# Performance work log

Hardware: AMD Instinct MI355X
Metric: run time of the kernel (lower is better)

The kernel has to match this reference:

```python
import jax, jax.numpy as jnp
import numpy as np

B, S = 8, 512          # batch, seq_len
D, F = 1024, 2048      # d_model, head hidden dim
H = 16                 # num_tasks (= num heads)
V = 3000               # selfies vocab
O = 1                  # head output size
INIT = 0.02


def setup_inputs() -> dict:
    key = jax.random.key(0)
    ks = jax.random.split(key, 12)
    return {
        "selfies": jax.random.randint(ks[0], (B, S), 0, V),
        "tasks": jax.random.randint(ks[1], (B, S), 0, H + 1),  # 0 -> invalid (-1)
        "values": jax.random.normal(ks[2], (B, S), jnp.float32),
        "property_mask": jax.random.randint(ks[3], (B, S), 0, 2).astype(bool),
        # shared_base params (embed + FFN -> [B,S,D])
        "emb_selfies": jax.random.normal(ks[4], (V, D), jnp.float32) * INIT,
        "emb_tasks": jax.random.normal(ks[5], (H + 1, D), jnp.float32) * INIT,
        "val_vec": jax.random.normal(ks[6], (D,), jnp.float32) * INIT,
        "Ws": jax.random.normal(ks[7], (D, D), jnp.float32) * INIT,
        "bs": jnp.zeros((D,), jnp.float32),
        # stacked per-head MLP params: Linear(D,F) -> GELU -> Linear(F,O)
        "W1": jax.random.normal(ks[8], (H, D, F), jnp.float32) * INIT,
        "b1": jnp.zeros((H, F), jnp.float32),
        "W2": jax.random.normal(ks[9], (H, F, O), jnp.float32) * INIT,
        "b2": jnp.zeros((H, O), jnp.float32),
    }


def reference(selfies, tasks, values, property_mask,
              emb_selfies, emb_tasks, val_vec, Ws, bs, W1, b1, W2, b2):
    # ---- shared_base: embed + masked token features + FFN -> [B,S,D] ----
    h = (emb_selfies[selfies] + emb_tasks[tasks] + values[..., None] * val_vec)
    h = h * property_mask[..., None].astype(h.dtype)
    shared = jax.nn.gelu(h @ Ws + bs)                      # [B,S,D]

    # ---- routing: task token -> head index, 0 means invalid (-1) ----
    head_idx = jnp.where(tasks > 0, (tasks - 1) % H, -1)   # [B,S]

    # ---- each active head runs its MLP over the FULL shared_output ----
    hid = jax.nn.gelu(jnp.einsum('bsd,hdf->bshf', shared, W1) + b1)  # [B,S,H,F]
    heads_out = jnp.einsum('bshf,hfo->bsho', hid, W2) + b2           # [B,S,H,O]

    # ---- scatter/select per token by head index; invalid -> zeros ----
    idx = jnp.clip(head_idx, 0)
    out = jnp.take_along_axis(heads_out, idx[..., None, None], axis=2)[:, :, 0, :]
    return jnp.where(head_idx[..., None] >= 0, out, jnp.zeros_like(out))
```

## Files before the change

kernel.cpp:

```cpp
#include <hip/hip_runtime.h>
#include <hip/hip_bf16.h>

#define TOK 4096
#define DD  1024
#define FF  2048
#define NH  16

typedef short bf16x8 __attribute__((ext_vector_type(8)));
typedef float f32x4  __attribute__((ext_vector_type(4)));

__device__ __forceinline__ float gelu_f(float x) {
  float u = 0.7978845608028654f * (x + 0.044715f * x * x * x);
  float e = __expf(2.0f * u);
  return 0.5f * x * (2.0f - 2.0f / (e + 1.0f));
}

__device__ __forceinline__ unsigned short f2bf(float f) {
  union { float f; unsigned u; } v; v.f = f;
  unsigned r = v.u + 0x7FFF + ((v.u >> 16) & 1);
  return (unsigned short)(r >> 16);
}
__device__ __forceinline__ unsigned pack2(float a, float b) {
  return (unsigned)f2bf(a) | ((unsigned)f2bf(b) << 16);
}

__device__ __forceinline__ void load_lds16(const void* g, void* l) {
  __builtin_amdgcn_global_load_lds(
      (const __attribute__((address_space(1))) void*)g,
      (__attribute__((address_space(3))) void*)l, 16, 0, 0);
}

__global__ __launch_bounds__(256) void route_kernel(
    const int* __restrict__ tasks, const float* __restrict__ b2,
    int* __restrict__ counts, int* __restrict__ lists, float* __restrict__ out) {
  int t = blockIdx.x * 256 + threadIdx.x;
  if (t >= TOK) return;
  int task = tasks[t];
  if (task > 0) {
    int h = (task - 1) & (NH - 1);
    int pos = atomicAdd(&counts[h], 1);
    lists[h * TOK + pos] = t;
    out[t] = b2[h];
  } else {
    out[t] = 0.0f;
  }
}

__global__ __launch_bounds__(256) void prep_x(
    const int* __restrict__ selfies, const int* __restrict__ tasks,
    const float* __restrict__ values, const int* __restrict__ pmask,
    const float* __restrict__ emb_s, const float* __restrict__ emb_t,
    const float* __restrict__ val_vec, unsigned short* __restrict__ Xb) {
  int gid = blockIdx.x * 256 + threadIdx.x;
  int kc = (gid & 127) * 8;
  int t  = gid >> 7;
  int sid = selfies[t], tsk = tasks[t];
  float v = values[t];
  float msk = pmask[t] ? 1.0f : 0.0f;
  const float* ps = emb_s + (size_t)sid * DD + kc;
  const float* pt = emb_t + (size_t)tsk * DD + kc;
  const float* pv = val_vec + kc;
  float r[8];
#pragma unroll
  for (int j = 0; j < 8; j += 4) {
    float4 a = *(const float4*)(ps + j);
    float4 b = *(const float4*)(pt + j);
    float4 c = *(const float4*)(pv + j);
    r[j + 0] = (a.x + b.x + v * c.x) * msk;
    r[j + 1] = (a.y + b.y + v * c.y) * msk;
    r[j + 2] = (a.z + b.z + v * c.z) * msk;
    r[j + 3] = (a.w + b.w + v * c.w) * msk;
  }
  uint4 o;
  o.x = pack2(r[0], r[1]); o.y = pack2(r[2], r[3]);
  o.z = pack2(r[4], r[5]); o.w = pack2(r[6], r[7]);
  *(uint4*)(Xb + (size_t)gid * 8) = o;
}

#define W1_TILES (16 * 16 * 32)
#define WS_TILES (16 * 16)

__global__ __launch_bounds__(256) void prep_w(
    const float* __restrict__ Ws, const float* __restrict__ W1,
    unsigned short* __restrict__ Wsp, unsigned short* __restrict__ W1p) {
  __shared__ unsigned short T[64][70];
  int bid = blockIdx.x;
  const float* src; unsigned short* dstBase; int stride, nt0, kc0;
  if (bid < W1_TILES) {
    int fb = bid & 31, kb = (bid >> 5) & 15, h = bid >> 9;
    src = W1 + ((size_t)h * DD + kb * 64) * FF + fb * 64;
    stride = FF;
    nt0 = h * 128 + fb * 4;
    kc0 = kb * 2;
    dstBase = W1p;
  } else {
    int b2 = bid - W1_TILES;
    int fb = b2 & 15, kb = b2 >> 4;
    src = Ws + (size_t)(kb * 64) * DD + fb * 64;
    stride = DD;
    nt0 = fb * 4;
    kc0 = kb * 2;
    dstBase = Wsp;
  }
  const int tid = threadIdx.x;
  {
    int r = tid >> 2, cq = (tid & 3) * 16;
    const float* p = src + (size_t)r * stride + cq;
#pragma unroll
    for (int i = 0; i < 4; ++i) {
      float4 v = *(const float4*)(p + i * 4);
      *(unsigned*)&T[r][cq + i * 4 + 0] = pack2(v.x, v.y);
      *(unsigned*)&T[r][cq + i * 4 + 2] = pack2(v.z, v.w);
    }
  }
  __syncthreads();
#pragma unroll
  for (int cc = 0; cc < 2; ++cc) {
    int idx = tid + cc * 256;
    int lane2 = idx & 63, kcl = (idx >> 6) & 1, ntl = idx >> 7;
    int n_local = ntl * 16 + (lane2 & 15);
    int r0 = kcl * 32 + (lane2 >> 4) * 8;
    unsigned short e[8];
#pragma unroll
    for (int j = 0; j < 8; ++j) e[j] = T[r0 + j][n_local];
    uint4 o;
    o.x = (unsigned)e[0] | ((unsigned)e[1] << 16);
    o.y = (unsigned)e[2] | ((unsigned)e[3] << 16);
    o.z = (unsigned)e[4] | ((unsigned)e[5] << 16);
    o.w = (unsigned)e[6] | ((unsigned)e[7] << 16);
    size_t chunk = ((size_t)(nt0 + ntl) * 32 + (kc0 + kcl)) * 64 + lane2;
    *(uint4*)(dstBase + chunk * 8) = o;
  }
}

__global__ __launch_bounds__(256) void gemm1_mfma(
    const unsigned short* __restrict__ Xb, const unsigned short* __restrict__ Wsp,
    const float* __restrict__ bs, unsigned short* __restrict__ shared_bf) {
  __shared__ __align__(16) unsigned short As[2][2 * 4 * 64 * 8];
  __shared__ __align__(16) unsigned short Bs[2][2 * 8 * 64 * 8];

  const int tid = threadIdx.x;
  const int lane = tid & 63, w = tid >> 6;
  const int m0 = blockIdx.x * 64;
  const int n0 = blockIdx.y * 128;
  const int q = lane >> 4, c = lane & 15;

  const unsigned short* aSrc = Xb + (size_t)(m0 + w * 16 + c) * DD + q * 8;
  const unsigned short* bBase = Wsp + ((size_t)(blockIdx.y * 8 + w * 2)) * 32 * 512 + lane * 8;
  f32x4 acc[4][2] = {};

  float bsv[2];
  bsv[0] = bs[n0 + w * 32 + c];
  bsv[1] = bs[n0 + w * 32 + 16 + c];
  asm volatile("" :: "v"(bsv[0]), "v"(bsv[1]));

  auto stage = [&](int buf, int k0) {
    load_lds16(aSrc + k0,      As[buf] + (size_t)(0 * 256 + w * 64 + lane) * 8);
    load_lds16(aSrc + k0 + 32, As[buf] + (size_t)(1 * 256 + w * 64 + lane) * 8);
    const unsigned short* bk = bBase + k0 * 16;
#pragma unroll
    for (int i = 0; i < 4; ++i) {
      int kk = i >> 1, t = i & 1;
      load_lds16(bk + (size_t)t * 16384 + kk * 512,
                 Bs[buf] + (size_t)(kk * 8 + w * 2 + t) * 512 + lane * 8);
    }
  };
  auto compute = [&](int buf) {
#pragma unroll
    for (int kk = 0; kk < 2; ++kk) {
      bf16x8 a[4], b[2];
#pragma unroll
      for (int mt = 0; mt < 4; ++mt)
        a[mt] = *(const bf16x8*)(As[buf] + (size_t)((kk * 4 + mt) * 64 + lane) * 8);
#pragma unroll
      for (int t = 0; t < 2; ++t)
        b[t] = *(const bf16x8*)(Bs[buf] + (size_t)((kk * 8 + w * 2 + t) * 64 + lane) * 8);
#pragma unroll
      for (int mt = 0; mt < 4; ++mt)
#pragma unroll
        for (int t = 0; t < 2; ++t)
          acc[mt][t] = __builtin_amdgcn_mfma_f32_16x16x32_bf16(a[mt], b[t], acc[mt][t], 0, 0, 0);
    }
  };

  stage(0, 0);
  stage(1, 64);
  asm volatile("s_waitcnt vmcnt(6)" ::: "memory");
  __builtin_amdgcn_s_barrier();
  int cur = 0;
  for (int i = 0; i < 14; ++i) {
    compute(cur);
    asm volatile("" ::: "memory");
    __builtin_amdgcn_s_barrier();
    stage(cur, (i + 2) * 64);
    asm volatile("s_waitcnt vmcnt(6)" ::: "memory");
    __builtin_amdgcn_s_barrier();
    cur ^= 1;
  }
  compute(cur);
  asm volatile("s_waitcnt vmcnt(0)" ::: "memory");
  __builtin_amdgcn_s_barrier();
  compute(cur ^ 1);

#pragma unroll
  for (int mt = 0; mt < 4; ++mt)
#pragma unroll
    for (int t = 0; t < 2; ++t)
#pragma unroll
      for (int r = 0; r < 4; ++r) {
        int row = m0 + mt * 16 + q * 4 + r;
        int col = n0 + w * 32 + t * 16 + c;
        shared_bf[(size_t)row * DD + col] = f2bf(gelu_f(acc[mt][t][r] + bsv[t]));
      }
}

__global__ __launch_bounds__(256) void gemm2_mfma(
    const unsigned short* __restrict__ shared_bf, const unsigned short* __restrict__ W1p,
    const float* __restrict__ b1, const float* __restrict__ W2,
    const int* __restrict__ counts, const int* __restrict__ lists,
    float* __restrict__ out) {
  const int id = blockIdx.x;
  const int xcd = id & 7, local_ = id >> 3;
  const int h = xcd + 8 * (local_ >> 7);
  const int rest = local_ & 127;
  const int fc = rest & 15;
  const int m0 = (rest >> 4) * 64;
  const int nt_h = counts[h];
  if (m0 >= nt_h) return;

  __shared__ __align__(16) unsigned short As[2][2 * 4 * 64 * 8];
  __shared__ __align__(16) unsigned short Bs[2][2 * 8 * 64 * 8];
  __shared__ int   stok[64];
  __shared__ float red[4][68];

  const int tid = threadIdx.x;
  const int lane = tid & 63, w = tid >> 6;
  const int q = lane >> 4, c = lane & 15;

  if (tid < 64) {
    int i = m0 + tid;
    stok[tid] = (i < nt_h) ? lists[h * TOK + i] : -1;
  }
  __syncthreads();

  int tokr = stok[w * 16 + c];
  if (tokr < 0) tokr = 0;
  const unsigned short* aSrc = shared_bf + (size_t)tokr * DD + q * 8;
  const unsigned short* bBase =
      W1p + ((size_t)h * 128 + fc * 8 + w * 2) * 32 * 512 + lane * 8;

  f32x4 acc[4][2] = {};

  const float* b1h = b1 + (size_t)h * FF + fc * 128 + w * 32;
  const float* w2h = W2 + (size_t)h * FF + fc * 128 + w * 32;
  float b1v[2], w2v[2];
  b1v[0] = b1h[c];      b1v[1] = b1h[16 + c];
  w2v[0] = w2h[c];      w2v[1] = w2h[16 + c];
  asm volatile("" :: "v"(b1v[0]), "v"(b1v[1]), "v"(w2v[0]), "v"(w2v[1]));

  auto stage = [&](int buf, int k0) {
    load_lds16(aSrc + k0,      As[buf] + (size_t)(0 * 256 + w * 64 + lane) * 8);
    load_lds16(aSrc + k0 + 32, As[buf] + (size_t)(1 * 256 + w * 64 + lane) * 8);
    const unsigned short* bk = bBase + k0 * 16;
#pragma unroll
    for (int i = 0; i < 4; ++i) {
      int kk = i >> 1, t = i & 1;
      load_lds16(bk + (size_t)t * 16384 + kk * 512,
                 Bs[buf] + (size_t)(kk * 8 + w * 2 + t) * 512 + lane * 8);
    }
  };
  auto compute = [&](int buf) {
#pragma unroll
    for (int kk = 0; kk < 2; ++kk) {
      bf16x8 a[4], b[2];
#pragma unroll
      for (int mt = 0; mt < 4; ++mt)
        a[mt] = *(const bf16x8*)(As[buf] + (size_t)((kk * 4 + mt) * 64 + lane) * 8);
#pragma unroll
      for (int t = 0; t < 2; ++t)
        b[t] = *(const bf16x8*)(Bs[buf] + (size_t)((kk * 8 + w * 2 + t) * 64 + lane) * 8);
#pragma unroll
      for (int mt = 0; mt < 4; ++mt)
#pragma unroll
        for (int t = 0; t < 2; ++t)
          acc[mt][t] = __builtin_amdgcn_mfma_f32_16x16x32_bf16(a[mt], b[t], acc[mt][t], 0, 0, 0);
    }
  };

  stage(0, 0);
  stage(1, 64);
  asm volatile("s_waitcnt vmcnt(6)" ::: "memory");
  __builtin_amdgcn_s_barrier();
  int cur = 0;
  for (int i = 0; i < 14; ++i) {
    compute(cur);
    asm volatile("" ::: "memory");
    __builtin_amdgcn_s_barrier();
    stage(cur, (i + 2) * 64);
    asm volatile("s_waitcnt vmcnt(6)" ::: "memory");
    __builtin_amdgcn_s_barrier();
    cur ^= 1;
  }
  compute(cur);
  asm volatile("s_waitcnt vmcnt(0)" ::: "memory");
  __builtin_amdgcn_s_barrier();
  compute(cur ^ 1);

#pragma unroll
  for (int mt = 0; mt < 4; ++mt)
#pragma unroll
    for (int r = 0; r < 4; ++r) {
      float s = 0.0f;
#pragma unroll
      for (int t = 0; t < 2; ++t)
        s += gelu_f(acc[mt][t][r] + b1v[t]) * w2v[t];
      s += __shfl_xor(s, 1);
      s += __shfl_xor(s, 2);
      s += __shfl_xor(s, 4);
      s += __shfl_xor(s, 8);
      if (c == 0) red[w][mt * 16 + q * 4 + r] = s;
    }
  __syncthreads();

  if (tid < 64) {
    int t = stok[tid];
    if (t >= 0) {
      float s = red[0][tid] + red[1][tid] + red[2][tid] + red[3][tid];
      atomicAdd(&out[t], s);
    }
  }
}

extern "C" void kernel_launch(void* const* d_in, const int* in_sizes, int n_in,
                              void* d_out, int out_size, void* d_ws, size_t ws_size,
                              hipStream_t stream) {
  const int*   selfies = (const int*)d_in[0];
  const int*   tasks   = (const int*)d_in[1];
  const float* values  = (const float*)d_in[2];
  const int*   pmask   = (const int*)d_in[3];
  const float* emb_s   = (const float*)d_in[4];
  const float* emb_t   = (const float*)d_in[5];
  const float* val_vec = (const float*)d_in[6];
  const float* Ws      = (const float*)d_in[7];
  const float* bs      = (const float*)d_in[8];
  const float* W1      = (const float*)d_in[9];
  const float* b1      = (const float*)d_in[10];
  const float* W2      = (const float*)d_in[11];
  const float* b2      = (const float*)d_in[12];
  float* out = (float*)d_out;

  char* ws = (char*)d_ws;
  unsigned short* Xb        = (unsigned short*)ws;
  unsigned short* shared_bf = (unsigned short*)(ws + (8u << 20));
  unsigned short* Wsp       = (unsigned short*)(ws + (16u << 20));
  unsigned short* W1p       = (unsigned short*)(ws + (18u << 20));
  int* counts = (int*)(ws + (82u << 20));
  int* lists  = (int*)(ws + (82u << 20) + 256);

  hipMemsetAsync(counts, 0, NH * sizeof(int), stream);
  route_kernel<<<TOK / 256, 256, 0, stream>>>(tasks, b2, counts, lists, out);
  prep_x<<<TOK * 128 / 256, 256, 0, stream>>>(selfies, tasks, values, pmask,
                                              emb_s, emb_t, val_vec, Xb);
  prep_w<<<W1_TILES + WS_TILES, 256, 0, stream>>>(Ws, W1, Wsp, W1p);
  gemm1_mfma<<<dim3(TOK / 64, DD / 128), 256, 0, stream>>>(Xb, Wsp, bs, shared_bf);
  gemm2_mfma<<<2048, 256, 0, stream>>>(shared_bf, W1p, b1, W2,
                                       counts, lists, out);
}
```

Measured before the change: 320.2 us.

## Merge prep kernels into one launch and deepen GEMM pipelines to four stages

Fuses the routing, activation-prep and weight-prep kernels into a single launch that dispatches on block index, removing two kernel launches and their gaps. Both MFMA GEMMs switch from a 2-buffer, 64-wide K step to a 4-buffer, 32-wide K step with one barrier per iteration and loads issued two steps ahead. MFMA sections are wrapped in s_setprio to favour the math waves. The deeper ring hides more global latency but halves the work per barrier, and the LDS footprint stays the same.

```diff
diff --git a/kernel.cpp b/kernel.cpp
--- a/kernel.cpp
+++ b/kernel.cpp
@@ -30,61 +30,15 @@
       (__attribute__((address_space(3))) void*)l, 16, 0, 0);
 }
 
-__global__ __launch_bounds__(256) void route_kernel(
-    const int* __restrict__ tasks, const float* __restrict__ b2,
-    int* __restrict__ counts, int* __restrict__ lists, float* __restrict__ out) {
-  int t = blockIdx.x * 256 + threadIdx.x;
-  if (t >= TOK) return;
-  int task = tasks[t];
-  if (task > 0) {
-    int h = (task - 1) & (NH - 1);
-    int pos = atomicAdd(&counts[h], 1);
-    lists[h * TOK + pos] = t;
-    out[t] = b2[h];
-  } else {
-    out[t] = 0.0f;
-  }
-}
-
-__global__ __launch_bounds__(256) void prep_x(
-    const int* __restrict__ selfies, const int* __restrict__ tasks,
-    const float* __restrict__ values, const int* __restrict__ pmask,
-    const float* __restrict__ emb_s, const float* __restrict__ emb_t,
-    const float* __restrict__ val_vec, unsigned short* __restrict__ Xb) {
-  int gid = blockIdx.x * 256 + threadIdx.x;
-  int kc = (gid & 127) * 8;
-  int t  = gid >> 7;
-  int sid = selfies[t], tsk = tasks[t];
-  float v = values[t];
-  float msk = pmask[t] ? 1.0f : 0.0f;
-  const float* ps = emb_s + (size_t)sid * DD + kc;
-  const float* pt = emb_t + (size_t)tsk * DD + kc;
-  const float* pv = val_vec + kc;
-  float r[8];
-#pragma unroll
-  for (int j = 0; j < 8; j += 4) {
-    float4 a = *(const float4*)(ps + j);
-    float4 b = *(const float4*)(pt + j);
-    float4 c = *(const float4*)(pv + j);
-    r[j + 0] = (a.x + b.x + v * c.x) * msk;
-    r[j + 1] = (a.y + b.y + v * c.y) * msk;
-    r[j + 2] = (a.z + b.z + v * c.z) * msk;
-    r[j + 3] = (a.w + b.w + v * c.w) * msk;
-  }
-  uint4 o;
-  o.x = pack2(r[0], r[1]); o.y = pack2(r[2], r[3]);
-  o.z = pack2(r[4], r[5]); o.w = pack2(r[6], r[7]);
-  *(uint4*)(Xb + (size_t)gid * 8) = o;
-}
-
 #define W1_TILES (16 * 16 * 32)
 #define WS_TILES (16 * 16)
-
-__global__ __launch_bounds__(256) void prep_w(
-    const float* __restrict__ Ws, const float* __restrict__ W1,
+#define PW_BLKS  (W1_TILES + WS_TILES)
+#define PX_BLKS  (TOK * 128 / 256)
+
+__device__ void prep_w_body(
+    int bid, const float* __restrict__ Ws, const float* __restrict__ W1,
     unsigned short* __restrict__ Wsp, unsigned short* __restrict__ W1p) {
   __shared__ unsigned short T[64][70];
-  int bid = blockIdx.x;
   const float* src; unsigned short* dstBase; int stride, nt0, kc0;
   if (bid < W1_TILES) {
     int fb = bid & 31, kb = (bid >> 5) & 15, h = bid >> 9;
@@ -133,11 +87,72 @@
   }
 }
 
+__device__ void prep_x_body(
+    int gid, const int* __restrict__ selfies, const int* __restrict__ tasks,
+    const float* __restrict__ values, const int* __restrict__ pmask,
+    const float* __restrict__ emb_s, const float* __restrict__ emb_t,
+    const float* __restrict__ val_vec, unsigned short* __restrict__ Xb) {
+  int kc = (gid & 127) * 8;
+  int t  = gid >> 7;
+  int sid = selfies[t], tsk = tasks[t];
+  float v = values[t];
+  float msk = pmask[t] ? 1.0f : 0.0f;
+  const float* ps = emb_s + (size_t)sid * DD + kc;
+  const float* pt = emb_t + (size_t)tsk * DD + kc;
+  const float* pv = val_vec + kc;
+  float r[8];
+#pragma unroll
+  for (int j = 0; j < 8; j += 4) {
+    float4 a = *(const float4*)(ps + j);
+    float4 b = *(const float4*)(pt + j);
+    float4 c = *(const float4*)(pv + j);
+    r[j + 0] = (a.x + b.x + v * c.x) * msk;
+    r[j + 1] = (a.y + b.y + v * c.y) * msk;
+    r[j + 2] = (a.z + b.z + v * c.z) * msk;
+    r[j + 3] = (a.w + b.w + v * c.w) * msk;
+  }
+  uint4 o;
+  o.x = pack2(r[0], r[1]); o.y = pack2(r[2], r[3]);
+  o.z = pack2(r[4], r[5]); o.w = pack2(r[6], r[7]);
+  *(uint4*)(Xb + (size_t)gid * 8) = o;
+}
+
+__global__ __launch_bounds__(256) void prep_all(
+    const int* __restrict__ selfies, const int* __restrict__ tasks,
+    const float* __restrict__ values, const int* __restrict__ pmask,
+    const float* __restrict__ emb_s, const float* __restrict__ emb_t,
+    const float* __restrict__ val_vec, const float* __restrict__ Ws,
+    const float* __restrict__ W1, const float* __restrict__ b2,
+    unsigned short* __restrict__ Xb, unsigned short* __restrict__ Wsp,
+    unsigned short* __restrict__ W1p,
+    int* __restrict__ counts, int* __restrict__ lists, float* __restrict__ out) {
+  int bid = blockIdx.x;
+  if (bid < PW_BLKS) {
+    prep_w_body(bid, Ws, W1, Wsp, W1p);
+  } else if (bid < PW_BLKS + PX_BLKS) {
+    prep_x_body((bid - PW_BLKS) * 256 + threadIdx.x,
+                selfies, tasks, values, pmask, emb_s, emb_t, val_vec, Xb);
+  } else {
+    int t = (bid - PW_BLKS - PX_BLKS) * 256 + threadIdx.x;
+    if (t < TOK) {
+      int task = tasks[t];
+      if (task > 0) {
+        int h = (task - 1) & (NH - 1);
+        int pos = atomicAdd(&counts[h], 1);
+        lists[h * TOK + pos] = t;
+        out[t] = b2[h];
+      } else {
+        out[t] = 0.0f;
+      }
+    }
+  }
+}
+
 __global__ __launch_bounds__(256) void gemm1_mfma(
     const unsigned short* __restrict__ Xb, const unsigned short* __restrict__ Wsp,
     const float* __restrict__ bs, unsigned short* __restrict__ shared_bf) {
-  __shared__ __align__(16) unsigned short As[2][2 * 4 * 64 * 8];
-  __shared__ __align__(16) unsigned short Bs[2][2 * 8 * 64 * 8];
+  __shared__ __align__(16) unsigned short As[4][4 * 64 * 8];
+  __shared__ __align__(16) unsigned short Bs[4][8 * 64 * 8];
 
   const int tid = threadIdx.x;
   const int lane = tid & 63, w = tid >> 6;
@@ -154,53 +169,45 @@
   bsv[1] = bs[n0 + w * 32 + 16 + c];
   asm volatile("" :: "v"(bsv[0]), "v"(bsv[1]));
 
-  auto stage = [&](int buf, int k0) {
-    load_lds16(aSrc + k0,      As[buf] + (size_t)(0 * 256 + w * 64 + lane) * 8);
-    load_lds16(aSrc + k0 + 32, As[buf] + (size_t)(1 * 256 + w * 64 + lane) * 8);
-    const unsigned short* bk = bBase + k0 * 16;
-#pragma unroll
-    for (int i = 0; i < 4; ++i) {
-      int kk = i >> 1, t = i & 1;
-      load_lds16(bk + (size_t)t * 16384 + kk * 512,
-                 Bs[buf] + (size_t)(kk * 8 + w * 2 + t) * 512 + lane * 8);
-    }
+  auto stage = [&](int buf, int kc2) {
+    load_lds16(aSrc + kc2 * 32, As[buf] + (size_t)(w * 64 + lane) * 8);
+    const unsigned short* bk = bBase + kc2 * 512;
+    load_lds16(bk,            Bs[buf] + (size_t)((w * 2 + 0) * 64 + lane) * 8);
+    load_lds16(bk + 16384,    Bs[buf] + (size_t)((w * 2 + 1) * 64 + lane) * 8);
   };
   auto compute = [&](int buf) {
-#pragma unroll
-    for (int kk = 0; kk < 2; ++kk) {
-      bf16x8 a[4], b[2];
-#pragma unroll
-      for (int mt = 0; mt < 4; ++mt)
-        a[mt] = *(const bf16x8*)(As[buf] + (size_t)((kk * 4 + mt) * 64 + lane) * 8);
+    bf16x8 a[4], b[2];
+#pragma unroll
+    for (int mt = 0; mt < 4; ++mt)
+      a[mt] = *(const bf16x8*)(As[buf] + (size_t)(mt * 64 + lane) * 8);
+#pragma unroll
+    for (int t = 0; t < 2; ++t)
+      b[t] = *(const bf16x8*)(Bs[buf] + (size_t)((w * 2 + t) * 64 + lane) * 8);
+    __builtin_amdgcn_s_setprio(1);
+#pragma unroll
+    for (int mt = 0; mt < 4; ++mt)
 #pragma unroll
       for (int t = 0; t < 2; ++t)
-        b[t] = *(const bf16x8*)(Bs[buf] + (size_t)((kk * 8 + w * 2 + t) * 64 + lane) * 8);
-#pragma unroll
-      for (int mt = 0; mt < 4; ++mt)
-#pragma unroll
-        for (int t = 0; t < 2; ++t)
-          acc[mt][t] = __builtin_amdgcn_mfma_f32_16x16x32_bf16(a[mt], b[t], acc[mt][t], 0, 0, 0);
-    }
+        acc[mt][t] = __builtin_amdgcn_mfma_f32_16x16x32_bf16(a[mt], b[t], acc[mt][t], 0, 0, 0);
+    __builtin_amdgcn_s_setprio(0);
   };
 
   stage(0, 0);
-  stage(1, 64);
-  asm volatile("s_waitcnt vmcnt(6)" ::: "memory");
-  __builtin_amdgcn_s_barrier();
-  int cur = 0;
-  for (int i = 0; i < 14; ++i) {
-    compute(cur);
-    asm volatile("" ::: "memory");
-    __builtin_amdgcn_s_barrier();
-    stage(cur, (i + 2) * 64);
+  stage(1, 1);
+  for (int i = 0; i < 30; ++i) {
+    stage((i + 2) & 3, i + 2);
     asm volatile("s_waitcnt vmcnt(6)" ::: "memory");
     __builtin_amdgcn_s_barrier();
-    cur ^= 1;
-  }
-  compute(cur);
+    compute(i & 3);
+    asm volatile("" ::: "memory");
+  }
+  asm volatile("s_waitcnt vmcnt(3)" ::: "memory");
+  __builtin_amdgcn_s_barrier();
+  compute(2);
+  asm volatile("" ::: "memory");
   asm volatile("s_waitcnt vmcnt(0)" ::: "memory");
   __builtin_amdgcn_s_barrier();
-  compute(cur ^ 1);
+  compute(3);
 
 #pragma unroll
   for (int mt = 0; mt < 4; ++mt)
@@ -228,8 +235,8 @@
   const int nt_h = counts[h];
   if (m0 >= nt_h) return;
 
-  __shared__ __align__(16) unsigned short As[2][2 * 4 * 64 * 8];
-  __shared__ __align__(16) unsigned short Bs[2][2 * 8 * 64 * 8];
+  __shared__ __align__(16) unsigned short As[4][4 * 64 * 8];
+  __shared__ __align__(16) unsigned short Bs[4][8 * 64 * 8];
   __shared__ int   stok[64];
   __shared__ float red[4][68];
 
@@ -258,53 +265,45 @@
   w2v[0] = w2h[c];      w2v[1] = w2h[16 + c];
   asm volatile("" :: "v"(b1v[0]), "v"(b1v[1]), "v"(w2v[0]), "v"(w2v[1]));
 
-  auto stage = [&](int buf, int k0) {
-    load_lds16(aSrc + k0,      As[buf] + (size_t)(0 * 256 + w * 64 + lane) * 8);
-    load_lds16(aSrc + k0 + 32, As[buf] + (size_t)(1 * 256 + w * 64 + lane) * 8);
-    const unsigned short* bk = bBase + k0 * 16;
-#pragma unroll
-    for (int i = 0; i < 4; ++i) {
-      int kk = i >> 1, t = i & 1;
-      load_lds16(bk + (size_t)t * 16384 + kk * 512,
-                 Bs[buf] + (size_t)(kk * 8 + w * 2 + t) * 512 + lane * 8);
-    }
+  auto stage = [&](int buf, int kc2) {
+    load_lds16(aSrc + kc2 * 32, As[buf] + (size_t)(w * 64 + lane) * 8);
+    const unsigned short* bk = bBase + kc2 * 512;
+    load_lds16(bk,            Bs[buf] + (size_t)((w * 2 + 0) * 64 + lane) * 8);
+    load_lds16(bk + 16384,    Bs[buf] + (size_t)((w * 2 + 1) * 64 + lane) * 8);
   };
   auto compute = [&](int buf) {
-#pragma unroll
-    for (int kk = 0; kk < 2; ++kk) {
-      bf16x8 a[4], b[2];
-#pragma unroll
-      for (int mt = 0; mt < 4; ++mt)
-        a[mt] = *(const bf16x8*)(As[buf] + (size_t)((kk * 4 + mt) * 64 + lane) * 8);
+    bf16x8 a[4], b[2];
+#pragma unroll
+    for (int mt = 0; mt < 4; ++mt)
+      a[mt] = *(const bf16x8*)(As[buf] + (size_t)(mt * 64 + lane) * 8);
+#pragma unroll
+    for (int t = 0; t < 2; ++t)
+      b[t] = *(const bf16x8*)(Bs[buf] + (size_t)((w * 2 + t) * 64 + lane) * 8);
+    __builtin_amdgcn_s_setprio(1);
+#pragma unroll
+    for (int mt = 0; mt < 4; ++mt)
 #pragma unroll
       for (int t = 0; t < 2; ++t)
-        b[t] = *(const bf16x8*)(Bs[buf] + (size_t)((kk * 8 + w * 2 + t) * 64 + lane) * 8);
-#pragma unroll
-      for (int mt = 0; mt < 4; ++mt)
-#pragma unroll
-        for (int t = 0; t < 2; ++t)
-          acc[mt][t] = __builtin_amdgcn_mfma_f32_16x16x32_bf16(a[mt], b[t], acc[mt][t], 0, 0, 0);
-    }
+        acc[mt][t] = __builtin_amdgcn_mfma_f32_16x16x32_bf16(a[mt], b[t], acc[mt][t], 0, 0, 0);
+    __builtin_amdgcn_s_setprio(0);
   };
 
   stage(0, 0);
-  stage(1, 64);
-  asm volatile("s_waitcnt vmcnt(6)" ::: "memory");
-  __builtin_amdgcn_s_barrier();
-  int cur = 0;
-  for (int i = 0; i < 14; ++i) {
-    compute(cur);
-    asm volatile("" ::: "memory");
-    __builtin_amdgcn_s_barrier();
-    stage(cur, (i + 2) * 64);
+  stage(1, 1);
+  for (int i = 0; i < 30; ++i) {
+    stage((i + 2) & 3, i + 2);
     asm volatile("s_waitcnt vmcnt(6)" ::: "memory");
     __builtin_amdgcn_s_barrier();
-    cur ^= 1;
-  }
-  compute(cur);
+    compute(i & 3);
+    asm volatile("" ::: "memory");
+  }
+  asm volatile("s_waitcnt vmcnt(3)" ::: "memory");
+  __builtin_amdgcn_s_barrier();
+  compute(2);
+  asm volatile("" ::: "memory");
   asm volatile("s_waitcnt vmcnt(0)" ::: "memory");
   __builtin_amdgcn_s_barrier();
-  compute(cur ^ 1);
+  compute(3);
 
 #pragma unroll
   for (int mt = 0; mt < 4; ++mt)
@@ -358,10 +357,9 @@
   int* lists  = (int*)(ws + (82u << 20) + 256);
 
   hipMemsetAsync(counts, 0, NH * sizeof(int), stream);
-  route_kernel<<<TOK / 256, 256, 0, stream>>>(tasks, b2, counts, lists, out);
-  prep_x<<<TOK * 128 / 256, 256, 0, stream>>>(selfies, tasks, values, pmask,
-                                              emb_s, emb_t, val_vec, Xb);
-  prep_w<<<W1_TILES + WS_TILES, 256, 0, stream>>>(Ws, W1, Wsp, W1p);
+  prep_all<<<PW_BLKS + PX_BLKS + TOK / 256, 256, 0, stream>>>(
+      selfies, tasks, values, pmask, emb_s, emb_t, val_vec, Ws, W1, b2,
+      Xb, Wsp, W1p, counts, lists, out);
   gemm1_mfma<<<dim3(TOK / 64, DD / 128), 256, 0, stream>>>(Xb, Wsp, bs, shared_bf);
   gemm2_mfma<<<2048, 256, 0, stream>>>(shared_bf, W1p, b1, W2,
                                        counts, lists, out);
```

New measurement: 304.2 us. 1.05x faster.
